# Performance work log

Hardware: AMD Instinct MI355X
Metric: run time of the kernel (lower is better)

Reference implementation:

```python
import jax, jax.numpy as jnp
import numpy as np

B, S, H, NH, D = 2, 2048, 2048, 16, 128
SCALE = D ** -0.5


def _rotate_half(x):
    x1, x2 = jnp.split(x, 2, axis=-1)
    return jnp.concatenate([-x2, x1], axis=-1)


def setup_inputs() -> dict:
    key = jax.random.key(0)
    ks = jax.random.split(key, 6)
    hidden_states = jax.random.normal(ks[0], (B, S, H), dtype=jnp.float32)
    # causal additive mask (batch, 1, q_len, kv_len)
    causal = jnp.where(jnp.tril(jnp.ones((S, S), dtype=bool)), 0.0, -1e9).astype(jnp.float32)
    attention_mask = jnp.broadcast_to(causal[None, None], (B, 1, S, S))
    # standard RoPE tables, theta=10000
    inv_freq = 1.0 / (10000.0 ** (jnp.arange(0, D, 2, dtype=jnp.float32) / D))
    t = jnp.arange(S, dtype=jnp.float32)
    freqs = jnp.einsum('s,f->sf', t, inv_freq)
    emb = jnp.concatenate([freqs, freqs], axis=-1)  # (S, D)
    rope_cos = jnp.cos(emb)[None, None]  # (1,1,S,D)
    rope_sin = jnp.sin(emb)[None, None]
    w_std = H ** -0.5
    Wq = jax.random.normal(ks[1], (H, NH * D), dtype=jnp.float32) * w_std
    Wk = jax.random.normal(ks[2], (H, D), dtype=jnp.float32) * w_std
    Wv = jax.random.normal(ks[3], (H, D), dtype=jnp.float32) * w_std
    Wo = jax.random.normal(ks[4], (NH * D, H), dtype=jnp.float32) * ((NH * D) ** -0.5)
    return {
        'hidden_states': hidden_states,
        'attention_mask': attention_mask,
        'rope_cos': rope_cos,
        'rope_sin': rope_sin,
        'Wq': Wq, 'Wk': Wk, 'Wv': Wv, 'Wo': Wo,
    }


def reference(hidden_states, attention_mask, rope_cos, rope_sin, Wq, Wk, Wv, Wo):
    b, s, _ = hidden_states.shape
    q = (hidden_states @ Wq).reshape(b, s, NH, D).transpose(0, 2, 1, 3)  # (b,h,s,d)
    k = (hidden_states @ Wk)[:, None]  # (b,1,s,d) single shared KV head
    v = (hidden_states @ Wv)[:, None]
    # inline RoPE on q and the shared k
    q = q * rope_cos + _rotate_half(q) * rope_sin
    k = k * rope_cos + _rotate_half(k) * rope_sin
    k = k[:, 0]  # (b,s,d); broadcast over heads instead of expand
    v = v[:, 0]
    scores = jnp.einsum('bhqd,bkd->bhqk', q, k) * SCALE + attention_mask
    attn = jax.nn.softmax(scores.astype(jnp.float32), axis=-1).astype(q.dtype)
    out = jnp.einsum('bhqk,bkd->bhqd', attn, v)
    out = out.transpose(0, 2, 1, 3).reshape(b, s, NH * D)
    return out @ Wo
```

## Files before the change

### kernel.cpp

```cpp
#include <hip/hip_runtime.h>
#include <hip/hip_bf16.h>

#define NB 2
#define NS 2048
#define NHID 2048
#define NHEAD 16
#define ND 128
#define NM (NB*NS)

typedef __attribute__((ext_vector_type(8))) short s16x8;
typedef __attribute__((ext_vector_type(4))) float f32x4;
typedef unsigned long long ull;

__device__ __forceinline__ short f2bf(float x) {
  unsigned u = __float_as_uint(x);
  u = (u + 0x7fffu + ((u >> 16) & 1u)) >> 16;
  return (short)u;
}

__device__ __forceinline__ float fexp2(float x) {
  float r; asm("v_exp_f32 %0, %1" : "=v"(r) : "v"(x)); return r;
}
__device__ __forceinline__ unsigned cvtpk(float lo, float hi) {
  unsigned r; asm("v_cvt_pk_bf16_f32 %0, %1, %2" : "=v"(r) : "v"(lo), "v"(hi)); return r;
}

__device__ __forceinline__ int colmap(int wc, int ni) {
  return (ni < 2) ? (wc*32 + ni*16) : (64 + wc*32 + (ni-2)*16);
}

__device__ __forceinline__ void gload16(const short* g, short* l) {
  __builtin_amdgcn_global_load_lds(
      (const __attribute__((address_space(1))) void*)g,
      (__attribute__((address_space(3))) void*)l, 16, 0, 0);
}

__global__ __launch_bounds__(256) void cvt_f32_bf16(const float* __restrict__ src,
                                                    short* __restrict__ dst, int n4) {
  int i = blockIdx.x*256 + threadIdx.x;
  if (i >= n4) return;
  const float4 v = reinterpret_cast<const float4*>(src)[i];
  ull pk =
      (ull)(unsigned)cvtpk(v.x, v.y)
    | ((ull)(unsigned)cvtpk(v.z, v.w) << 32);
  reinterpret_cast<ull*>(dst)[i] = pk;
}

__global__ __launch_bounds__(256) void cvtT(const float* __restrict__ src,
                                            short* __restrict__ dst, int K, int N) {
  __shared__ float t[32][33];
  const int n0 = blockIdx.x*32, k0 = blockIdx.y*32;
  const int tx = threadIdx.x & 31, ty = threadIdx.x >> 5;
  #pragma unroll
  for (int i = 0; i < 4; ++i)
    t[ty + 8*i][tx] = src[(size_t)(k0 + ty + 8*i)*N + n0 + tx];
  __syncthreads();
  #pragma unroll
  for (int i = 0; i < 4; ++i)
    dst[(size_t)(n0 + ty + 8*i)*K + k0 + tx] = f2bf(t[tx][ty + 8*i]);
}

__global__ __launch_bounds__(256) void trans_v(const short* __restrict__ src,
                                               short* __restrict__ dst) {
  __shared__ short t[32][40];
  const int c0 = blockIdx.x*32;
  const int r0 = blockIdx.y*32;
  const int tx = threadIdx.x & 31, ty = threadIdx.x >> 5;
  #pragma unroll
  for (int i = 0; i < 4; ++i)
    t[ty + 8*i][tx] = src[(size_t)(r0 + ty + 8*i)*128 + c0 + tx];
  __syncthreads();
  #pragma unroll
  for (int i = 0; i < 4; ++i) {
    const int d = c0 + ty + 8*i;
    dst[(size_t)d*4096 + ((r0 + tx) ^ ((d & 7) << 3))] = t[tx][ty + 8*i];
  }
}

__global__ __launch_bounds__(256) void gemm_qkv(
    const short* __restrict__ hsb, const short* __restrict__ WqT,
    const short* __restrict__ WkT, const short* __restrict__ WvT,
    const float* __restrict__ ropeC, const float* __restrict__ ropeS,
    short* __restrict__ Qb, short* __restrict__ Kb, short* __restrict__ Vb)
{
  const int tid = threadIdx.x;
  const int lane = tid & 63, wid = tid >> 6;
  const int wr = wid >> 1, wc = wid & 1;
  const int l15 = lane & 15, l4 = lane >> 4;
  const int bid = blockIdx.x;
  const int wg = (bid & 7) * 72 + (bid >> 3);
  const int m0 = (wg & 31) * 128;
  const int ny = wg >> 5;
  const short* Bt = (ny < 16) ? (WqT + (size_t)ny*128*2048) : (ny == 16 ? WkT : WvT);

  __shared__ short Al[128][32];
  __shared__ short Bl[128][32];

  f32x4 acc[4][4];
  const f32x4 zf = {0.f,0.f,0.f,0.f};
  #pragma unroll
  for (int i=0;i<4;++i)
    #pragma unroll
    for (int j=0;j<4;++j) acc[i][j] = zf;

  const int srow = tid >> 2;
  const int scol = (tid & 3) * 8;
  const short* Ap0 = hsb + (size_t)(m0 + srow)*2048 + scol;
  const short* Ap1 = hsb + (size_t)(m0 + 64 + srow)*2048 + scol;
  const short* Bp0 = Bt + (size_t)srow*2048 + scol;
  const short* Bp1 = Bt + (size_t)(64 + srow)*2048 + scol;
  short* AL0 = &Al[0][0] + tid*8;
  short* AL1 = &Al[0][0] + 2048 + tid*8;
  short* BL0 = &Bl[0][0] + tid*8;
  short* BL1 = &Bl[0][0] + 2048 + tid*8;

  for (int kt = 0; kt < 64; ++kt) {
    const int k0 = kt * 32;
    __syncthreads();
    gload16(Ap0 + k0, AL0);
    gload16(Ap1 + k0, AL1);
    gload16(Bp0 + k0, BL0);
    gload16(Bp1 + k0, BL1);
    __syncthreads();
    s16x8 af[4], bfr[4];
    #pragma unroll
    for (int mi=0; mi<4; ++mi) af[mi] = *(const s16x8*)&Al[wr*64 + mi*16 + l15][l4*8];
    #pragma unroll
    for (int ni=0; ni<4; ++ni) bfr[ni] = *(const s16x8*)&Bl[colmap(wc,ni) + l15][l4*8];
    #pragma unroll
    for (int mi=0; mi<4; ++mi)
      #pragma unroll
      for (int ni=0; ni<4; ++ni)
        acc[mi][ni] = __builtin_amdgcn_mfma_f32_16x16x32_bf16(af[mi], bfr[ni], acc[mi][ni], 0,0,0);
  }

  const bool isQ = (ny < 16), isK = (ny == 16);
  #pragma unroll
  for (int mi=0; mi<4; ++mi) {
    #pragma unroll
    for (int r=0; r<4; ++r) {
      const int mrow = m0 + wr*64 + mi*16 + l4*4 + r;
      const int s = mrow & 2047;
      const int bb = mrow >> 11;
      if (!isQ && !isK) {
        #pragma unroll
        for (int ni=0; ni<4; ++ni) {
          const int d = colmap(wc,ni) + l15;
          Vb[(size_t)mrow*128 + d] = f2bf(acc[mi][ni][r]);
        }
      } else {
        #pragma unroll
        for (int ni=0; ni<2; ++ni) {
          const int d = colmap(wc,ni) + l15;
          const float c0 = ropeC[s*128 + d],      s0 = ropeS[s*128 + d];
          const float c1 = ropeC[s*128 + d + 64], s1 = ropeS[s*128 + d + 64];
          const float x0 = acc[mi][ni][r], x1 = acc[mi][ni+2][r];
          const float y0 = x0*c0 - x1*s0;
          const float y1 = x1*c1 + x0*s1;
          if (isK) {
            const int dsw = d ^ ((s & 7) << 3);
            Kb[(size_t)mrow*128 + dsw]      = f2bf(y0);
            Kb[(size_t)mrow*128 + dsw + 64] = f2bf(y1);
          } else {
            const size_t base = ((size_t)(bb*16 + ny)*2048 + s)*128;
            Qb[base + d]      = f2bf(y0);
            Qb[base + d + 64] = f2bf(y1);
          }
        }
      }
    }
  }
}

__device__ __forceinline__ void qkt_pair(const short* KL, const s16x8 (&qfH)[4],
                                         const s16x8 (&qfL)[4], f32x4 (&scH)[4],
                                         f32x4 (&scL)[4], int l15, int l4, int sw) {
  __builtin_amdgcn_s_setprio(1);
  #pragma unroll
  for (int kk=0; kk<4; ++kk)
    #pragma unroll
    for (int n=0; n<4; ++n) {
      s16x8 kf = *(const s16x8*)&KL[(n*16 + l15)*128 + ((kk*32 + l4*8) ^ sw)];
      scH[n] = __builtin_amdgcn_mfma_f32_16x16x32_bf16(kf, qfH[kk], scH[n], 0,0,0);
      scL[n] = __builtin_amdgcn_mfma_f32_16x16x32_bf16(kf, qfL[kk], scL[n], 0,0,0);
    }
  __builtin_amdgcn_s_setprio(0);
}

__device__ __forceinline__ void qkt_one(const short* KL, const s16x8 (&qf)[4],
                                        f32x4 (&sc)[4], int l15, int l4, int sw) {
  __builtin_amdgcn_s_setprio(1);
  #pragma unroll
  for (int kk=0; kk<4; ++kk)
    #pragma unroll
    for (int n=0; n<4; ++n) {
      s16x8 kf = *(const s16x8*)&KL[(n*16 + l15)*128 + ((kk*32 + l4*8) ^ sw)];
      sc[n] = __builtin_amdgcn_mfma_f32_16x16x32_bf16(kf, qf[kk], sc[n], 0,0,0);
    }
  __builtin_amdgcn_s_setprio(0);
}

__device__ __forceinline__ void sm16(f32x4 (&sc)[4], bool diag, int wid, int l15, int l4,
                                     int sw, float &m_run, float &l_run, f32x4 (&o)[8],
                                     short* Pl) {
  const float CEXP = 0.08838834764831845f * 1.44269504088896340f;
  float p[4][4];
  #pragma unroll
  for (int n=0;n<4;++n)
    #pragma unroll
    for (int r=0;r<4;++r) p[n][r] = sc[n][r];
  if (diag) {
    #pragma unroll
    for (int n=0;n<4;++n)
      #pragma unroll
      for (int r=0;r<4;++r)
        if (n*16 + l4*4 + r > wid*16 + l15) p[n][r] = -1e30f;
  }
  float a0 = fmaxf(fmaxf(p[0][0], p[0][1]), p[0][2]);
  float a1 = fmaxf(fmaxf(p[0][3], p[1][0]), p[1][1]);
  float a2 = fmaxf(fmaxf(p[1][2], p[1][3]), p[2][0]);
  float a3 = fmaxf(fmaxf(p[2][1], p[2][2]), p[2][3]);
  float a4 = fmaxf(fmaxf(p[3][0], p[3][1]), p[3][2]);
  float b0 = fmaxf(fmaxf(a0, a1), a2);
  float b1 = fmaxf(fmaxf(a3, a4), p[3][3]);
  float pm = fmaxf(b0, b1);
  pm = fmaxf(pm, __shfl_xor(pm, 16));
  pm = fmaxf(pm, __shfl_xor(pm, 32));

  if (!__all(pm <= m_run + 8.0f)) {
    const float mn = fmaxf(m_run, pm);
    const float al = fexp2((m_run - mn) * CEXP);
    m_run = mn;
    l_run *= al;
    #pragma unroll
    for (int r=0;r<4;++r) {
      const float a = __shfl(al, l4*4 + r);
      #pragma unroll
      for (int i=0;i<8;++i) o[i][r] *= a;
    }
  }
  const float mC = m_run * CEXP;
  #pragma unroll
  for (int n=0;n<4;++n)
    #pragma unroll
    for (int r=0;r<4;++r)
      p[n][r] = fexp2(__builtin_fmaf(p[n][r], CEXP, -mC));
  #pragma unroll
  for (int n=0;n<4;++n) {
    ull w = (ull)(unsigned)cvtpk(p[n][0], p[n][1])
          | ((ull)(unsigned)cvtpk(p[n][2], p[n][3]) << 32);
    *(ull*)&Pl[l15*64 + ((n*16 + l4*4) ^ sw)] = w;
  }
  float rs = 0.f;
  #pragma unroll
  for (int n=0;n<4;++n)
    #pragma unroll
    for (int r=0;r<4;++r) rs += p[n][r];
  rs += __shfl_xor(rs, 16);
  rs += __shfl_xor(rs, 32);
  l_run += rs;
}

__device__ __forceinline__ void pv_pair(const short* VL, const s16x8 (&paH)[2],
                                        const s16x8 (&paL)[2], f32x4 (&oH)[8],
                                        f32x4 (&oL)[8], int l15, int l4, int sw) {
  __builtin_amdgcn_s_setprio(1);
  #pragma unroll
  for (int kb=0; kb<2; ++kb)
    #pragma unroll
    for (int d8=0; d8<8; ++d8) {
      s16x8 vf = *(const s16x8*)&VL[(d8*16 + l15)*64 + ((kb*32 + l4*8) ^ sw)];
      oH[d8] = __builtin_amdgcn_mfma_f32_16x16x32_bf16(paH[kb], vf, oH[d8], 0,0,0);
      oL[d8] = __builtin_amdgcn_mfma_f32_16x16x32_bf16(paL[kb], vf, oL[d8], 0,0,0);
    }
  __builtin_amdgcn_s_setprio(0);
}

__device__ __forceinline__ void pv_one(const short* VL, const s16x8 (&pa)[2],
                                       f32x4 (&o)[8], int l15, int l4, int sw) {
  __builtin_amdgcn_s_setprio(1);
  #pragma unroll
  for (int kb=0; kb<2; ++kb)
    #pragma unroll
    for (int d8=0; d8<8; ++d8) {
      s16x8 vf = *(const s16x8*)&VL[(d8*16 + l15)*64 + ((kb*32 + l4*8) ^ sw)];
      o[d8] = __builtin_amdgcn_mfma_f32_16x16x32_bf16(pa[kb], vf, o[d8], 0,0,0);
    }
  __builtin_amdgcn_s_setprio(0);
}

__global__ __launch_bounds__(256) void attn_fwd(
    const short* __restrict__ Qb, const short* __restrict__ Kb,
    const short* __restrict__ VbT, short* __restrict__ Ob)
{
  const int tid = threadIdx.x;
  const int lane = tid & 63, wid = tid >> 6;
  const int l15 = lane & 15, l4 = lane >> 4;
  const int bid = blockIdx.x;
  const int wg = (bid & 7)*64 + (bid >> 3);
  const int pr = wg & 15, h = (wg >> 4) & 15, b = wg >> 8;
  const int lo = pr, hi = 31 - pr;
  const int sw = (l15 & 7) << 3;

  __shared__ short Kl[2][64*128];
  __shared__ short Vt[2][128*64];
  __shared__ short Pb[4][2][16*64];
  short* PlH = &Pb[wid][0][0];
  short* PlL = &Pb[wid][1][0];

  s16x8 qfH[4], qfL[4];
  {
    const short* QpL = Qb + ((size_t)(b*16 + h)*2048 + lo*64 + wid*16 + l15)*128 + l4*8;
    const short* QpH = Qb + ((size_t)(b*16 + h)*2048 + hi*64 + wid*16 + l15)*128 + l4*8;
    #pragma unroll
    for (int kk=0; kk<4; ++kk) { qfL[kk] = *(const s16x8*)(QpL + kk*32);
                                 qfH[kk] = *(const s16x8*)(QpH + kk*32); }
  }

  float mH = -1e30f, lH = 0.f, mL = -1e30f, lL = 0.f;
  f32x4 oH[8], oL[8];
  const f32x4 zf = {0.f,0.f,0.f,0.f};
  #pragma unroll
  for (int i=0;i<8;++i){ oH[i]=zf; oL[i]=zf; }

  const short* Kg = Kb + (size_t)b*2048*128;
  const short* Vg = VbT + (size_t)b*2048;

  #define STAGE(bufi, tt) do {                                              \
    const int kv0_ = (tt)*64;                                               \
    _Pragma("unroll")                                                       \
    for (int rep=0; rep<4; ++rep) {                                         \
      const int c = tid + rep*256;                                          \
      gload16(Kg + (size_t)(kv0_ + (c>>4))*128 + (c&15)*8, &Kl[bufi][c*8]); \
    }                                                                       \
    _Pragma("unroll")                                                       \
    for (int rep=0; rep<4; ++rep) {                                         \
      const int c = tid + rep*256;                                          \
      gload16(Vg + (size_t)(c>>3)*4096 + kv0_ + (c&7)*8, &Vt[bufi][c*8]);   \
    }                                                                       \
  } while(0)

  STAGE(0, 0);
  __syncthreads();
  int buf = 0;
  int t = 0;

  for (; t <= lo; ++t) {
    STAGE(buf^1, t+1);
    const short* KL = &Kl[buf][0];
    const short* VL = &Vt[buf][0];
    f32x4 scH[4], scL[4];
    #pragma unroll
    for (int n=0;n<4;++n){ scH[n]=zf; scL[n]=zf; }
    qkt_pair(KL, qfH, qfL, scH, scL, l15, l4, sw);
    sm16(scH, false, wid, l15, l4, sw, mH, lH, oH, PlH);
    sm16(scL, (t == lo), wid, l15, l4, sw, mL, lL, oL, PlL);
    s16x8 paH[2], paL[2];
    #pragma unroll
    for (int kb=0; kb<2; ++kb) {
      paH[kb] = *(const s16x8*)&PlH[l15*64 + ((kb*32 + l4*8) ^ sw)];
      paL[kb] = *(const s16x8*)&PlL[l15*64 + ((kb*32 + l4*8) ^ sw)];
    }
    pv_pair(VL, paH, paL, oH, oL, l15, l4, sw);
    __syncthreads();
    buf ^= 1;
  }
  for (; t <= hi; ++t) {
    if (t < hi) STAGE(buf^1, t+1);
    const short* KL = &Kl[buf][0];
    const short* VL = &Vt[buf][0];
    f32x4 scH[4];
    #pragma unroll
    for (int n=0;n<4;++n) scH[n]=zf;
    qkt_one(KL, qfH, scH, l15, l4, sw);
    sm16(scH, (t == hi), wid, l15, l4, sw, mH, lH, oH, PlH);
    s16x8 paH[2];
    #pragma unroll
    for (int kb=0; kb<2; ++kb)
      paH[kb] = *(const s16x8*)&PlH[l15*64 + ((kb*32 + l4*8) ^ sw)];
    pv_one(VL, paH, oH, l15, l4, sw);
    __syncthreads();
    buf ^= 1;
  }
  #undef STAGE

  const float invH = 1.0f / lH;
  const float invL = 1.0f / lL;
  #pragma unroll
  for (int r=0;r<4;++r) {
    const float iH = __shfl(invH, l4*4 + r);
    const float iL = __shfl(invL, l4*4 + r);
    const size_t baseH = ((size_t)(b*2048) + hi*64 + wid*16 + l4*4 + r)*2048 + (size_t)h*128;
    const size_t baseL = ((size_t)(b*2048) + lo*64 + wid*16 + l4*4 + r)*2048 + (size_t)h*128;
    #pragma unroll
    for (int d8=0; d8<8; ++d8) {
      Ob[baseH + d8*16 + l15] = f2bf(oH[d8][r] * iH);
      Ob[baseL + d8*16 + l15] = f2bf(oL[d8][r] * iL);
    }
  }
}

__global__ __launch_bounds__(256) void gemm_out(
    const short* __restrict__ Ob, const short* __restrict__ WoT,
    float* __restrict__ out)
{
  const int tid = threadIdx.x;
  const int lane = tid & 63, wid = tid >> 6;
  const int wr = wid >> 1, wc = wid & 1;
  const int l15 = lane & 15, l4 = lane >> 4;
  const int bid = blockIdx.x;
  const int wg = (bid & 7) * 64 + (bid >> 3);
  const int m0 = (wg & 31) * 128;
  const int n0 = (wg >> 5) * 128;

  __shared__ short Al[128][32];
  __shared__ short Bl[128][32];

  f32x4 acc[4][4];
  const f32x4 zf = {0.f,0.f,0.f,0.f};
  #pragma unroll
  for (int i=0;i<4;++i)
    #pragma unroll
    for (int j=0;j<4;++j) acc[i][j] = zf;

  const int srow = tid >> 2;
  const int scol = (tid & 3) * 8;
  const short* Ap0 = Ob + (size_t)(m0 + srow)*2048 + scol;
  const short* Ap1 = Ob + (size_t)(m0 + 64 + srow)*2048 + scol;
  const short* Bp0 = WoT + (size_t)(n0 + srow)*2048 + scol;
  const short* Bp1 = WoT + (size_t)(n0 + 64 + srow)*2048 + scol;
  short* AL0 = &Al[0][0] + tid*8;
  short* AL1 = &Al[0][0] + 2048 + tid*8;
  short* BL0 = &Bl[0][0] + tid*8;
  short* BL1 = &Bl[0][0] + 2048 + tid*8;

  for (int kt = 0; kt < 64; ++kt) {
    const int k0 = kt * 32;
    __syncthreads();
    gload16(Ap0 + k0, AL0);
    gload16(Ap1 + k0, AL1);
    gload16(Bp0 + k0, BL0);
    gload16(Bp1 + k0, BL1);
    __syncthreads();
    s16x8 af[4], bfr[4];
    #pragma unroll
    for (int mi=0; mi<4; ++mi) af[mi] = *(const s16x8*)&Al[wr*64 + mi*16 + l15][l4*8];
    #pragma unroll
    for (int ni=0; ni<4; ++ni) bfr[ni] = *(const s16x8*)&Bl[colmap(wc,ni) + l15][l4*8];
    #pragma unroll
    for (int mi=0; mi<4; ++mi)
      #pragma unroll
      for (int ni=0; ni<4; ++ni)
        acc[mi][ni] = __builtin_amdgcn_mfma_f32_16x16x32_bf16(af[mi], bfr[ni], acc[mi][ni], 0,0,0);
  }

  #pragma unroll
  for (int mi=0; mi<4; ++mi)
    #pragma unroll
    for (int r=0; r<4; ++r) {
      const int mrow = m0 + wr*64 + mi*16 + l4*4 + r;
      #pragma unroll
      for (int ni=0; ni<4; ++ni)
        out[(size_t)mrow*2048 + n0 + colmap(wc,ni) + l15] = acc[mi][ni][r];
    }
}

extern "C" void kernel_launch(void* const* d_in, const int* in_sizes, int n_in,
                              void* d_out, int out_size, void* d_ws, size_t ws_size,
                              hipStream_t stream) {
  const float* hidden = (const float*)d_in[0];
  const float* ropeC  = (const float*)d_in[2];
  const float* ropeS  = (const float*)d_in[3];
  const float* Wq     = (const float*)d_in[4];
  const float* Wk     = (const float*)d_in[5];
  const float* Wv     = (const float*)d_in[6];
  const float* Wo     = (const float*)d_in[7];
  float* out = (float*)d_out;
  char* ws = (char*)d_ws;

  short* hsb = (short*)(ws + 0);
  short* WqT = (short*)(ws + 16777216);
  short* WkT = (short*)(ws + 25165824);
  short* WvT = (short*)(ws + 25690112);
  short* WoT = (short*)(ws + 26214400);
  short* Qb  = (short*)(ws + 34603008);
  short* Kb  = (short*)(ws + 51380224);
  short* Vb  = (short*)(ws + 52428800);
  short* VbT = (short*)(ws + 53477376);
  short* Ob  = hsb;

  cvt_f32_bf16<<<dim3((NM*NHID/4 + 255)/256), dim3(256), 0, stream>>>(hidden, hsb, NM*NHID/4);
  cvtT<<<dim3(64,64), dim3(256), 0, stream>>>(Wq, WqT, 2048, 2048);
  cvtT<<<dim3(4, 64), dim3(256), 0, stream>>>(Wk, WkT, 2048, 128);
  cvtT<<<dim3(4, 64), dim3(256), 0, stream>>>(Wv, WvT, 2048, 128);
  cvtT<<<dim3(64,64), dim3(256), 0, stream>>>(Wo, WoT, 2048, 2048);

  gemm_qkv<<<dim3(576), dim3(256), 0, stream>>>(hsb, WqT, WkT, WvT, ropeC, ropeS, Qb, Kb, Vb);
  trans_v<<<dim3(4, 128), dim3(256), 0, stream>>>(Vb, VbT);
  attn_fwd<<<dim3(512), dim3(256), 0, stream>>>(Qb, Kb, VbT, Ob);
  gemm_out<<<dim3(512), dim3(256), 0, stream>>>(Ob, WoT, out);
}
```

Measured before the change: 410.0 us.

## Double GEMM K-tile to 64 with XOR-swizzled LDS and reordered tile mapping

Both the QKV and output projection GEMMs now stage a 64-wide K slice per iteration instead of 32. This halves the number of barrier pairs and loop iterations. LDS rows are XOR-swizzled by row index, both on the direct global-to-LDS load and on the fragment reads, to avoid bank conflicts from the wider 128-byte rows. The block-to-tile mapping is also changed so neighbouring blocks share an M tile and walk across N, which alters L2 reuse. LDS usage doubles per block, which may reduce occupancy.

```diff
diff --git a/kernel.cpp b/kernel.cpp
--- a/kernel.cpp
+++ b/kernel.cpp
@@ -89,12 +89,12 @@
   const int l15 = lane & 15, l4 = lane >> 4;
   const int bid = blockIdx.x;
   const int wg = (bid & 7) * 72 + (bid >> 3);
-  const int m0 = (wg & 31) * 128;
-  const int ny = wg >> 5;
+  const int m0 = (wg / 18) * 128;
+  const int ny = wg % 18;
   const short* Bt = (ny < 16) ? (WqT + (size_t)ny*128*2048) : (ny == 16 ? WkT : WvT);
 
-  __shared__ short Al[128][32];
-  __shared__ short Bl[128][32];
+  __shared__ short Al[128][64];
+  __shared__ short Bl[128][64];
 
   f32x4 acc[4][4];
   const f32x4 zf = {0.f,0.f,0.f,0.f};
@@ -103,35 +103,35 @@
     #pragma unroll
     for (int j=0;j<4;++j) acc[i][j] = zf;
 
-  const int srow = tid >> 2;
-  const int scol = (tid & 3) * 8;
-  const short* Ap0 = hsb + (size_t)(m0 + srow)*2048 + scol;
-  const short* Ap1 = hsb + (size_t)(m0 + 64 + srow)*2048 + scol;
-  const short* Bp0 = Bt + (size_t)srow*2048 + scol;
-  const short* Bp1 = Bt + (size_t)(64 + srow)*2048 + scol;
-  short* AL0 = &Al[0][0] + tid*8;
-  short* AL1 = &Al[0][0] + 2048 + tid*8;
-  short* BL0 = &Bl[0][0] + tid*8;
-  short* BL1 = &Bl[0][0] + 2048 + tid*8;
-
-  for (int kt = 0; kt < 64; ++kt) {
-    const int k0 = kt * 32;
+  const int sw7 = l15 & 7;
+
+  for (int kt = 0; kt < 32; ++kt) {
+    const int k0 = kt * 64;
     __syncthreads();
-    gload16(Ap0 + k0, AL0);
-    gload16(Ap1 + k0, AL1);
-    gload16(Bp0 + k0, BL0);
-    gload16(Bp1 + k0, BL1);
+    #pragma unroll
+    for (int rep=0; rep<4; ++rep) {
+      const int idx = rep*256 + tid;
+      const int row = idx >> 3;
+      const int qs  = (idx & 7) ^ (row & 7);
+      gload16(hsb + (size_t)(m0+row)*2048 + k0 + qs*8, &Al[0][0] + idx*8);
+      gload16(Bt  + (size_t)row*2048      + k0 + qs*8, &Bl[0][0] + idx*8);
+    }
     __syncthreads();
-    s16x8 af[4], bfr[4];
-    #pragma unroll
-    for (int mi=0; mi<4; ++mi) af[mi] = *(const s16x8*)&Al[wr*64 + mi*16 + l15][l4*8];
-    #pragma unroll
-    for (int ni=0; ni<4; ++ni) bfr[ni] = *(const s16x8*)&Bl[colmap(wc,ni) + l15][l4*8];
-    #pragma unroll
-    for (int mi=0; mi<4; ++mi)
+    #pragma unroll
+    for (int kk=0; kk<2; ++kk) {
+      s16x8 af[4], bfr[4];
+      #pragma unroll
+      for (int mi=0; mi<4; ++mi)
+        af[mi] = *(const s16x8*)&Al[0][0 + (wr*64 + mi*16 + l15)*64 + (((kk*4 + l4) ^ sw7) * 8)];
       #pragma unroll
       for (int ni=0; ni<4; ++ni)
-        acc[mi][ni] = __builtin_amdgcn_mfma_f32_16x16x32_bf16(af[mi], bfr[ni], acc[mi][ni], 0,0,0);
+        bfr[ni] = *(const s16x8*)&Bl[0][0 + (colmap(wc,ni) + l15)*64 + (((kk*4 + l4) ^ sw7) * 8)];
+      #pragma unroll
+      for (int mi=0; mi<4; ++mi)
+        #pragma unroll
+        for (int ni=0; ni<4; ++ni)
+          acc[mi][ni] = __builtin_amdgcn_mfma_f32_16x16x32_bf16(af[mi], bfr[ni], acc[mi][ni], 0,0,0);
+    }
   }
 
   const bool isQ = (ny < 16), isK = (ny == 16);
@@ -410,11 +410,11 @@
   const int l15 = lane & 15, l4 = lane >> 4;
   const int bid = blockIdx.x;
   const int wg = (bid & 7) * 64 + (bid >> 3);
-  const int m0 = (wg & 31) * 128;
-  const int n0 = (wg >> 5) * 128;
-
-  __shared__ short Al[128][32];
-  __shared__ short Bl[128][32];
+  const int m0 = (wg >> 4) * 128;
+  const int n0 = (wg & 15) * 128;
+
+  __shared__ short Al[128][64];
+  __shared__ short Bl[128][64];
 
   f32x4 acc[4][4];
   const f32x4 zf = {0.f,0.f,0.f,0.f};
@@ -423,35 +423,35 @@
     #pragma unroll
     for (int j=0;j<4;++j) acc[i][j] = zf;
 
-  const int srow = tid >> 2;
-  const int scol = (tid & 3) * 8;
-  const short* Ap0 = Ob + (size_t)(m0 + srow)*2048 + scol;
-  const short* Ap1 = Ob + (size_t)(m0 + 64 + srow)*2048 + scol;
-  const short* Bp0 = WoT + (size_t)(n0 + srow)*2048 + scol;
-  const short* Bp1 = WoT + (size_t)(n0 + 64 + srow)*2048 + scol;
-  short* AL0 = &Al[0][0] + tid*8;
-  short* AL1 = &Al[0][0] + 2048 + tid*8;
-  short* BL0 = &Bl[0][0] + tid*8;
-  short* BL1 = &Bl[0][0] + 2048 + tid*8;
-
-  for (int kt = 0; kt < 64; ++kt) {
-    const int k0 = kt * 32;
+  const int sw7 = l15 & 7;
+
+  for (int kt = 0; kt < 32; ++kt) {
+    const int k0 = kt * 64;
     __syncthreads();
-    gload16(Ap0 + k0, AL0);
-    gload16(Ap1 + k0, AL1);
-    gload16(Bp0 + k0, BL0);
-    gload16(Bp1 + k0, BL1);
+    #pragma unroll
+    for (int rep=0; rep<4; ++rep) {
+      const int idx = rep*256 + tid;
+      const int row = idx >> 3;
+      const int qs  = (idx & 7) ^ (row & 7);
+      gload16(Ob  + (size_t)(m0+row)*2048 + k0 + qs*8, &Al[0][0] + idx*8);
+      gload16(WoT + (size_t)(n0+row)*2048 + k0 + qs*8, &Bl[0][0] + idx*8);
+    }
     __syncthreads();
-    s16x8 af[4], bfr[4];
-    #pragma unroll
-    for (int mi=0; mi<4; ++mi) af[mi] = *(const s16x8*)&Al[wr*64 + mi*16 + l15][l4*8];
-    #pragma unroll
-    for (int ni=0; ni<4; ++ni) bfr[ni] = *(const s16x8*)&Bl[colmap(wc,ni) + l15][l4*8];
-    #pragma unroll
-    for (int mi=0; mi<4; ++mi)
+    #pragma unroll
+    for (int kk=0; kk<2; ++kk) {
+      s16x8 af[4], bfr[4];
+      #pragma unroll
+      for (int mi=0; mi<4; ++mi)
+        af[mi] = *(const s16x8*)&Al[0][0 + (wr*64 + mi*16 + l15)*64 + (((kk*4 + l4) ^ sw7) * 8)];
       #pragma unroll
       for (int ni=0; ni<4; ++ni)
-        acc[mi][ni] = __builtin_amdgcn_mfma_f32_16x16x32_bf16(af[mi], bfr[ni], acc[mi][ni], 0,0,0);
+        bfr[ni] = *(const s16x8*)&Bl[0][0 + (colmap(wc,ni) + l15)*64 + (((kk*4 + l4) ^ sw7) * 8)];
+      #pragma unroll
+      for (int mi=0; mi<4; ++mi)
+        #pragma unroll
+        for (int ni=0; ni<4; ++ni)
+          acc[mi][ni] = __builtin_amdgcn_mfma_f32_16x16x32_bf16(af[mi], bfr[ni], acc[mi][ni], 0,0,0);
+    }
   }
 
   #pragma unroll
```

Result: faster. 374.8 us (-8.6%).
